# Kernel tuning notes

Measured on AMD Instinct MI355X. Metric: run time of the kernel, lower is better.

The kernel has to match this reference:

```python
import jax, jax.numpy as jnp
import numpy as np
import math

N_ENTITIES = 200000
N_ITEMS = 100000
N_REL = 40
DIM = 64
N_HEADS = 2
DK = DIM // N_HEADS
N_EDGES = 1500000
K_EDGES = 256
K_ITEMS = 100


def setup_inputs() -> dict:
    key = jax.random.key(0)
    k1, k2, k3, k4, k5, k6 = jax.random.split(key, 6)
    entity_emb = jax.random.normal(k1, (N_ENTITIES, DIM), jnp.float32) * 0.1
    W_Q = jax.random.normal(k2, (DIM, DIM), jnp.float32) * (1.0 / math.sqrt(DIM))
    relation_emb = jax.random.normal(k3, (N_REL - 1, DIM), jnp.float32) * 0.1
    edge_index = jax.random.randint(k4, (2, N_EDGES), 0, N_ENTITIES, jnp.int32)
    # edge_type in [1, N_REL-1]: code indexes relation_emb[edge_type - 1]
    edge_type = jax.random.randint(k5, (N_EDGES,), 1, N_REL, jnp.int32)
    # uniform(0,1) driving the gumbel noise -log(-log(u)); clipped away from 0
    noise_u = jax.random.uniform(k6, (N_EDGES,), jnp.float32, 1e-9, 1.0)
    return {"entity_emb": entity_emb, "W_Q": W_Q, "relation_emb": relation_emb,
            "noise_u": noise_u, "edge_index": edge_index, "edge_type": edge_type}


def reference(entity_emb, W_Q, relation_emb, noise_u, edge_index, edge_type):
    head, tail = edge_index[0], edge_index[1]
    E = edge_index.shape[1]

    # --- norm_attn_computer (AttnHGCN): per-edge multi-head attention ---
    # project once on nodes, then gather (same math as (emb[head] @ W_Q))
    proj = entity_emb @ W_Q                               # [N, D]
    q = proj[head].reshape(E, N_HEADS, DK)                # [E, H, Dk]
    k = proj[tail].reshape(E, N_HEADS, DK)                # [E, H, Dk]
    rel = relation_emb[edge_type - 1].reshape(E, N_HEADS, DK)
    attn = jnp.sum(q * k * rel, axis=-1) / math.sqrt(DK)  # [E, H]
    edge_attn_logits = attn.mean(axis=-1)                 # [E]

    # scatter_softmax over head nodes, then multiply by head degree (norm)
    seg_max = jax.lax.stop_gradient(
        jax.ops.segment_max(edge_attn_logits, head, num_segments=N_ENTITIES))
    ex = jnp.exp(edge_attn_logits - seg_max[head])
    denom = jax.ops.segment_sum(ex, head, num_segments=N_ENTITIES)
    edge_attn_score = ex / denom[head]
    deg = jax.ops.segment_sum(jnp.ones_like(edge_attn_logits), head,
                              num_segments=N_ENTITIES)
    edge_attn_score = edge_attn_score * deg[head]         # [E]

    # --- attn logit sums per item (head + tail scatter_sum), topk 100 ---
    sum_by_node = (jax.ops.segment_sum(edge_attn_logits, head, num_segments=N_ENTITIES)
                   + jax.ops.segment_sum(edge_attn_logits, tail, num_segments=N_ENTITIES))
    top_items_v, top_attn_items = jax.lax.top_k(sum_by_node[:N_ITEMS], K_ITEMS)

    # --- gumbel-noise injection + edge topk 256 ---
    noisy_score = edge_attn_score + (-jnp.log(-jnp.log(noise_u)))
    topk_v, topk_attn_edge_id = jax.lax.top_k(noisy_score, K_EDGES)

    return (edge_attn_score, topk_v, topk_attn_edge_id, top_items_v, top_attn_items)
```

## Files before the change

kernel.cpp:

```cpp
#include <hip/hip_runtime.h>

#define N_ENTITIES 200000
#define N_ITEMS    100000
#define DIM        64
#define N_EDGES    1500000
#define K_EDGES    256
#define K_ITEMS    100
#define SCALE      0.08838834764831845f

#define CAND_CAP   8192
#define NBLK3      1024

typedef unsigned long long u64;


__device__ __forceinline__ unsigned fkey(float x) {
    unsigned u = __float_as_uint(x);
    return (u & 0x80000000u) ? ~u : (u | 0x80000000u);
}
__device__ __forceinline__ float funkey(unsigned k) {
    return (k & 0x80000000u) ? __uint_as_float(k & 0x7fffffffu)
                             : __uint_as_float(~k);
}

__device__ __forceinline__ unsigned select_digit(const unsigned* __restrict__ hist,
                                                 unsigned Keff, unsigned* above) {
    unsigned cum = 0;
    int b = 255;
    for (; b > 0; --b) {
        unsigned hb = hist[b];
        if (cum + hb >= Keff) break;
        cum += hb;
    }
    *above = cum;
    return (unsigned)b;
}

__global__ __launch_bounds__(256) void proj_kernel(const float* __restrict__ emb,
                                                   const float* __restrict__ W,
                                                   float* __restrict__ proj,
                                                   const int* __restrict__ head,
                                                   float* __restrict__ ndf) {
    int e = blockIdx.x * blockDim.x + threadIdx.x;
    if (e < N_EDGES) atomicAdd(&ndf[2 * head[e] + 1], 1.0f);

    __shared__ float part[4][16][64];
    const int t = threadIdx.x;
    const int c = t & 63;
    const int q = __builtin_amdgcn_readfirstlane(t >> 6);

    float Wreg[16];
#pragma unroll
    for (int j = 0; j < 16; ++j) Wreg[j] = W[(q * 16 + j) * 64 + c];

    const int base = blockIdx.x * 16;
    const float* erow = emb + (size_t)base * 64 + q * 16;

    float acc[16];
#pragma unroll
    for (int r = 0; r < 16; ++r) acc[r] = 0.f;
#pragma unroll
    for (int r = 0; r < 16; ++r) {
#pragma unroll
        for (int j = 0; j < 16; ++j)
            acc[r] += erow[r * 64 + j] * Wreg[j];
    }
#pragma unroll
    for (int r = 0; r < 16; ++r) part[q][r][c] = acc[r];
    __syncthreads();
#pragma unroll
    for (int it = 0; it < 4; ++it) {
        int oi = t + it * 256;
        int r = oi >> 6, cc = oi & 63;
        float s = part[0][r][cc] + part[1][r][cc] + part[2][r][cc] + part[3][r][cc];
        proj[(size_t)(base + r) * 64 + cc] = s;
    }
}

__global__ __launch_bounds__(256) void edge_main(const float4* __restrict__ proj4,
                                                 const float4* __restrict__ rel4,
                                                 const int* __restrict__ head,
                                                 const int* __restrict__ tail,
                                                 const int* __restrict__ etype,
                                                 float* __restrict__ logits,
                                                 float* __restrict__ ndf,
                                                 float* __restrict__ sumI) {
    int wave = (blockIdx.x * blockDim.x + threadIdx.x) >> 6;
    int lane = threadIdx.x & 63;
    int slot = lane >> 4, sl = lane & 15;
    int ea = wave * 8 + slot, eb = ea + 4;

    int ha  = head[ea],  hb  = head[eb];
    int tta = tail[ea],  ttb = tail[eb];
    int ria = etype[ea] - 1, rib = etype[eb] - 1;

    float4 pha = proj4[(size_t)ha  * 16 + sl];
    float4 pta = proj4[(size_t)tta * 16 + sl];
    float4 qra = rel4[(size_t)ria * 16 + sl];
    float4 phb = proj4[(size_t)hb  * 16 + sl];
    float4 ptb = proj4[(size_t)ttb * 16 + sl];
    float4 qrb = rel4[(size_t)rib * 16 + sl];

    float xa = pha.x * pta.x * qra.x + pha.y * pta.y * qra.y
             + pha.z * pta.z * qra.z + pha.w * pta.w * qra.w;
    float xb = phb.x * ptb.x * qrb.x + phb.y * ptb.y * qrb.y
             + phb.z * ptb.z * qrb.z + phb.w * ptb.w * qrb.w;
    xa += __shfl_xor(xa, 1, 64);  xb += __shfl_xor(xb, 1, 64);
    xa += __shfl_xor(xa, 2, 64);  xb += __shfl_xor(xb, 2, 64);
    xa += __shfl_xor(xa, 4, 64);  xb += __shfl_xor(xb, 4, 64);
    xa += __shfl_xor(xa, 8, 64);  xb += __shfl_xor(xb, 8, 64);

    if (sl == 0) {
        float lga = xa * SCALE, lgb = xb * SCALE;
        logits[ea] = lga;
        logits[eb] = lgb;
        atomicAdd(&ndf[2 * ha], __expf(lga));
        atomicAdd(&ndf[2 * hb], __expf(lgb));
        if (ha  < N_ITEMS) atomicAdd(&sumI[ha],  lga);
        if (tta < N_ITEMS) atomicAdd(&sumI[tta], lga);
        if (hb  < N_ITEMS) atomicAdd(&sumI[hb],  lgb);
        if (ttb < N_ITEMS) atomicAdd(&sumI[ttb], lgb);
    }
}

__global__ __launch_bounds__(256) void edge_pass3(const float* __restrict__ logits,
                           const int* __restrict__ head,
                           const float* __restrict__ ndf, const float* __restrict__ noise_u,
                           const float* __restrict__ sumI,
                           float* __restrict__ out_scores, unsigned* __restrict__ keysE,
                           unsigned* __restrict__ keysI, unsigned* __restrict__ histB) {
    __shared__ unsigned hh[512];
    for (int j = threadIdx.x; j < 512; j += blockDim.x) hh[j] = 0;
    __syncthreads();

    const int stride = NBLK3 * 256;
    for (int i = blockIdx.x * blockDim.x + threadIdx.x; i < N_EDGES; i += stride) {
        float lg = logits[i];
        float2 dd = ((const float2*)ndf)[head[i]];
        float score = __expf(lg) / dd.x * dd.y;
        out_scores[i] = score;
        float noise = -logf(-logf(noise_u[i]));
        unsigned k = fkey(score + noise);
        keysE[i] = k;
        atomicAdd(&hh[k >> 24], 1u);
        if (i < N_ITEMS) {
            unsigned ki = fkey(sumI[i]);
            keysI[i] = ki;
            atomicAdd(&hh[256 + (ki >> 24)], 1u);
        }
    }
    __syncthreads();
    unsigned* row = histB + (size_t)blockIdx.x * 512;
    for (int j = threadIdx.x; j < 512; j += blockDim.x) row[j] = hh[j];
}

__global__ void reduce_hist_kernel(const unsigned* __restrict__ histB,
                                   unsigned* __restrict__ hists) {
    const int bin = blockIdx.x;
    unsigned s = 0;
    for (int r = threadIdx.x; r < NBLK3; r += 64)
        s += histB[(size_t)r * 512 + bin];
#pragma unroll
    for (int off = 1; off < 64; off <<= 1) s += __shfl_xor(s, off, 64);
    if (threadIdx.x == 0) hists[bin] = s;
}

__global__ void collect_kernel(const unsigned* __restrict__ keysE,
                               const unsigned* __restrict__ keysI,
                               const unsigned* __restrict__ hists,
                               unsigned* __restrict__ counters, unsigned* __restrict__ cand) {
    const int y = blockIdx.y;
    const unsigned* keys = y ? keysI : keysE;
    const int n = y ? N_ITEMS : N_EDGES;
    const unsigned K = y ? K_ITEMS : K_EDGES;
    const unsigned* H = hists + (size_t)y * 256;
    unsigned aboveA;
    unsigned binA = select_digit(H, K, &aboveA);
    const unsigned T = binA << 24;
    unsigned* cd = cand + (size_t)y * 2 * CAND_CAP;

    int i = blockIdx.x * blockDim.x + threadIdx.x;
    int stride = gridDim.x * blockDim.x;
    for (; i < n; i += stride) {
        unsigned k = keys[i];
        if (k >= T) {
            unsigned p = atomicAdd(&counters[y], 1u);
            if (p < (unsigned)CAND_CAP) { cd[2 * p] = k; cd[2 * p + 1] = (unsigned)i; }
        }
    }
}

__global__ void final_topk_kernel(const unsigned* __restrict__ cand,
                                  const unsigned* __restrict__ counters,
                                  float* __restrict__ out_topkv, float* __restrict__ out_topki,
                                  float* __restrict__ out_itemv, float* __restrict__ out_itemi) {
    __shared__ unsigned sk[CAND_CAP];
    __shared__ unsigned si[CAND_CAP];
    const int y = blockIdx.x;
    const int K = y ? K_ITEMS : K_EDGES;
    float* outv = y ? out_itemv : out_topkv;
    float* outi = y ? out_itemi : out_topki;
    const unsigned* cd = cand + (size_t)y * 2 * CAND_CAP;
    unsigned m = counters[y];
    if (m > (unsigned)CAND_CAP) m = CAND_CAP;
    for (unsigned i = threadIdx.x; i < m; i += blockDim.x) {
        sk[i] = cd[2 * i];
        si[i] = cd[2 * i + 1];
    }
    __syncthreads();
    for (unsigned i = threadIdx.x; i < m; i += blockDim.x) {
        unsigned ki = sk[i], xi = si[i];
        int r = 0;
        for (unsigned j = 0; j < m; ++j) {
            unsigned kj = sk[j];
            if (kj > ki || (kj == ki && si[j] < xi)) r++;
        }
        if (r < K) {
            outv[r] = funkey(ki);
            outi[r] = (float)xi;
        }
    }
}

extern "C" void kernel_launch(void* const* d_in, const int* in_sizes, int n_in,
                              void* d_out, int out_size, void* d_ws, size_t ws_size,
                              hipStream_t stream) {
    (void)in_sizes; (void)n_in; (void)out_size; (void)ws_size;
    const float* emb    = (const float*)d_in[0];
    const float* W      = (const float*)d_in[1];
    const float* rel    = (const float*)d_in[2];
    const float* noise  = (const float*)d_in[3];
    const int*   eidx   = (const int*)d_in[4];
    const int*   etype  = (const int*)d_in[5];
    const int* head = eidx;
    const int* tail = eidx + N_EDGES;

    float* out        = (float*)d_out;
    float* out_scores = out;
    float* out_topkv  = out + N_EDGES;
    float* out_topki  = out + N_EDGES + K_EDGES;
    float* out_itemv  = out + N_EDGES + 2 * K_EDGES;
    float* out_itemi  = out + N_EDGES + 2 * K_EDGES + K_ITEMS;

    float* ws = (float*)d_ws;
    size_t o = 0;
    float*    proj    = ws + o;               o += (size_t)N_ENTITIES * DIM;
    float*    ndf     = ws + o;               o += 2 * (size_t)N_ENTITIES;
    float*    sumI    = ws + o;               o += N_ITEMS;
    unsigned* counters= (unsigned*)(ws + o);  o += 2;
    float*    logits  = ws + o;               o += N_EDGES;
    unsigned* keysE   = (unsigned*)(ws + o);  o += N_EDGES;
    unsigned* keysI   = (unsigned*)(ws + o);  o += N_ITEMS;
    unsigned* histB   = (unsigned*)(ws + o);  o += (size_t)NBLK3 * 512;
    unsigned* hists   = (unsigned*)(ws + o);  o += 512;
    unsigned* cand    = (unsigned*)(ws + o);  o += 2 * 2 * CAND_CAP;

    hipMemsetAsync(ndf, 0, (2 * (size_t)N_ENTITIES + N_ITEMS + 2) * 4, stream);
    hipLaunchKernelGGL(proj_kernel, dim3(12500), dim3(256), 0, stream,
                       emb, W, proj, head, ndf);
    hipLaunchKernelGGL(edge_main, dim3(46875), dim3(256), 0, stream,
                       (const float4*)proj, (const float4*)rel, head, tail, etype,
                       logits, ndf, sumI);
    hipLaunchKernelGGL(edge_pass3, dim3(NBLK3), dim3(256), 0, stream,
                       logits, head, ndf, noise, sumI,
                       out_scores, keysE, keysI, histB);
    hipLaunchKernelGGL(reduce_hist_kernel, dim3(512), dim3(64), 0, stream, histB, hists);
    hipLaunchKernelGGL(collect_kernel, dim3(512, 2), dim3(256), 0, stream,
                       keysE, keysI, hists, counters, cand);
    hipLaunchKernelGGL(final_topk_kernel, dim3(2), dim3(1024), 0, stream,
                       cand, counters, out_topkv, out_topki, out_itemv, out_itemi);
}
```

Before: 476.1 us.

## Build head-sorted CSR via two-level bucket sort and process edges per node

Replaces per-edge processing with a counting sort of edges by head node: a two-level radix (bucket hist, scan, scatter, then per-bucket local sort in shared memory) produces a CSR of packed 64-bit edge records. A per-node wave kernel then loads the head projection once, computes logits for all outgoing edges, and accumulates softmax denominator, degree and head logit sums in registers instead of global atomics. This removes the head-indexed atomics and repeated head-row gathers, but adds five extra kernels and extra global traffic for the sort. Bucket capacity is clamped at L2CAP, so an unusually large bucket would silently drop edges.

```diff
diff --git a/kernel.cpp b/kernel.cpp
--- a/kernel.cpp
+++ b/kernel.cpp
@@ -10,6 +10,11 @@
 
 #define CAND_CAP   8192
 #define NBLK3      1024
+#define NB1        256
+#define EPB        5860
+#define NBUCK      782
+#define NSC        (NBUCK * NB1)
+#define L2CAP      2816
 
 typedef unsigned long long u64;
 
@@ -38,12 +43,7 @@
 
 __global__ __launch_bounds__(256) void proj_kernel(const float* __restrict__ emb,
                                                    const float* __restrict__ W,
-                                                   float* __restrict__ proj,
-                                                   const int* __restrict__ head,
-                                                   float* __restrict__ ndf) {
-    int e = blockIdx.x * blockDim.x + threadIdx.x;
-    if (e < N_EDGES) atomicAdd(&ndf[2 * head[e] + 1], 1.0f);
-
+                                                   float* __restrict__ proj) {
     __shared__ float part[4][16][64];
     const int t = threadIdx.x;
     const int c = t & 63;
@@ -77,56 +77,193 @@
     }
 }
 
-__global__ __launch_bounds__(256) void edge_main(const float4* __restrict__ proj4,
+__global__ __launch_bounds__(256) void bhist_kernel(const int* __restrict__ head,
+                                                    unsigned* __restrict__ off) {
+    __shared__ unsigned lh[NBUCK];
+    for (int k = threadIdx.x; k < NBUCK; k += 256) lh[k] = 0;
+    __syncthreads();
+    int base = blockIdx.x * EPB;
+    int end = base + EPB; if (end > N_EDGES) end = N_EDGES;
+    for (int e = base + threadIdx.x; e < end; e += 256)
+        atomicAdd(&lh[(unsigned)head[e] >> 8], 1u);
+    __syncthreads();
+    for (int k = threadIdx.x; k < NBUCK; k += 256)
+        off[(size_t)k * NB1 + blockIdx.x] = lh[k];
+}
+
+__global__ void scanA_kernel(unsigned* __restrict__ a, unsigned* __restrict__ bsum) {
+    __shared__ unsigned s[256];
+    int t = threadIdx.x, i = blockIdx.x * 256 + t;
+    unsigned v = a[i];
+    s[t] = v;
+    __syncthreads();
+    for (int off = 1; off < 256; off <<= 1) {
+        unsigned x = s[t];
+        unsigned y = (t >= off) ? s[t - off] : 0u;
+        __syncthreads();
+        s[t] = x + y;
+        __syncthreads();
+    }
+    a[i] = s[t] - v;
+    if (t == 255) bsum[blockIdx.x] = s[t];
+}
+__global__ __launch_bounds__(256) void scanB_kernel(const unsigned* __restrict__ bsum,
+                                                    unsigned* __restrict__ a) {
+    __shared__ unsigned part[4];
+    const int b = blockIdx.x;
+    const int t = threadIdx.x;
+    unsigned s = 0;
+    for (int j = t; j < b; j += 256) s += bsum[j];
+#pragma unroll
+    for (int off = 1; off < 64; off <<= 1) s += __shfl_xor(s, off, 64);
+    if ((t & 63) == 0) part[t >> 6] = s;
+    __syncthreads();
+    unsigned prefix = part[0] + part[1] + part[2] + part[3];
+    a[b * 256 + t] += prefix;
+}
+
+__global__ __launch_bounds__(256) void bscat_kernel(const int* __restrict__ head,
+                                                    const int* __restrict__ tail,
+                                                    const int* __restrict__ etype,
+                                                    const unsigned* __restrict__ off,
+                                                    u64* __restrict__ rec2) {
+    __shared__ unsigned lh[NBUCK];
+    __shared__ unsigned loff[NBUCK];
+    for (int k = threadIdx.x; k < NBUCK; k += 256) {
+        lh[k] = 0;
+        loff[k] = off[(size_t)k * NB1 + blockIdx.x];
+    }
+    __syncthreads();
+    int base = blockIdx.x * EPB;
+    int end = base + EPB; if (end > N_EDGES) end = N_EDGES;
+    for (int e = base + threadIdx.x; e < end; e += 256) {
+        unsigned h = (unsigned)head[e];
+        unsigned bkt = h >> 8;
+        unsigned r = atomicAdd(&lh[bkt], 1u);
+        u64 R = ((u64)h << 45) | ((u64)(unsigned)tail[e] << 27)
+              | ((u64)(unsigned)(etype[e] - 1) << 21) | (u64)(unsigned)e;
+        rec2[loff[bkt] + r] = R;
+    }
+}
+
+__global__ __launch_bounds__(256) void csr_kernel(const u64* __restrict__ rec2,
+                                                  const unsigned* __restrict__ off,
+                                                  u64* __restrict__ rec3,
+                                                  unsigned* __restrict__ start,
+                                                  unsigned* __restrict__ degtot) {
+    __shared__ u64 srec[L2CAP];
+    __shared__ u64 sdst[L2CAP];
+    __shared__ unsigned short srank[L2CAP];
+    __shared__ unsigned lh[256];
+    __shared__ unsigned lscan[256];
+    const int bkt = blockIdx.x;
+    const unsigned gstart = off[(size_t)bkt * NB1];
+    const unsigned gend = (bkt == NBUCK - 1) ? (unsigned)N_EDGES
+                                             : off[(size_t)(bkt + 1) * NB1];
+    unsigned n = gend - gstart;
+    if (n > L2CAP) n = L2CAP;
+    lh[threadIdx.x] = 0;
+    __syncthreads();
+    for (unsigned j = threadIdx.x; j < n; j += 256) {
+        u64 R = rec2[gstart + j];
+        srec[j] = R;
+        unsigned hl = (unsigned)(R >> 45) & 255u;
+        srank[j] = (unsigned short)atomicAdd(&lh[hl], 1u);
+    }
+    __syncthreads();
+    unsigned v = lh[threadIdx.x];
+    lscan[threadIdx.x] = v;
+    __syncthreads();
+    for (int o = 1; o < 256; o <<= 1) {
+        unsigned x = lscan[threadIdx.x];
+        unsigned y = (threadIdx.x >= o) ? lscan[threadIdx.x - o] : 0u;
+        __syncthreads();
+        lscan[threadIdx.x] = x + y;
+        __syncthreads();
+    }
+    unsigned excl = lscan[threadIdx.x] - v;
+    __syncthreads();
+    lscan[threadIdx.x] = excl;
+    const int h0 = bkt * 256;
+    const int entCount = (N_ENTITIES - h0 < 256) ? (N_ENTITIES - h0) : 256;
+    if ((int)threadIdx.x < entCount) {
+        start[h0 + threadIdx.x] = gstart + excl;
+        degtot[h0 + threadIdx.x] = v;
+    }
+    __syncthreads();
+    for (unsigned j = threadIdx.x; j < n; j += 256) {
+        u64 R = srec[j];
+        unsigned hl = (unsigned)(R >> 45) & 255u;
+        sdst[lscan[hl] + srank[j]] = R;
+    }
+    __syncthreads();
+    for (unsigned j = threadIdx.x; j < n; j += 256) rec3[gstart + j] = sdst[j];
+}
+
+__global__ __launch_bounds__(256) void node_pass(const float4* __restrict__ proj4,
                                                  const float4* __restrict__ rel4,
-                                                 const int* __restrict__ head,
-                                                 const int* __restrict__ tail,
-                                                 const int* __restrict__ etype,
+                                                 const u64* __restrict__ rec,
+                                                 const unsigned* __restrict__ start,
+                                                 const unsigned* __restrict__ degtot,
                                                  float* __restrict__ logits,
-                                                 float* __restrict__ ndf,
+                                                 float2* __restrict__ nd,
+                                                 float* __restrict__ sumhead,
                                                  float* __restrict__ sumI) {
     int wave = (blockIdx.x * blockDim.x + threadIdx.x) >> 6;
     int lane = threadIdx.x & 63;
     int slot = lane >> 4, sl = lane & 15;
-    int ea = wave * 8 + slot, eb = ea + 4;
-
-    int ha  = head[ea],  hb  = head[eb];
-    int tta = tail[ea],  ttb = tail[eb];
-    int ria = etype[ea] - 1, rib = etype[eb] - 1;
-
-    float4 pha = proj4[(size_t)ha  * 16 + sl];
-    float4 pta = proj4[(size_t)tta * 16 + sl];
-    float4 qra = rel4[(size_t)ria * 16 + sl];
-    float4 phb = proj4[(size_t)hb  * 16 + sl];
-    float4 ptb = proj4[(size_t)ttb * 16 + sl];
-    float4 qrb = rel4[(size_t)rib * 16 + sl];
-
-    float xa = pha.x * pta.x * qra.x + pha.y * pta.y * qra.y
-             + pha.z * pta.z * qra.z + pha.w * pta.w * qra.w;
-    float xb = phb.x * ptb.x * qrb.x + phb.y * ptb.y * qrb.y
-             + phb.z * ptb.z * qrb.z + phb.w * ptb.w * qrb.w;
-    xa += __shfl_xor(xa, 1, 64);  xb += __shfl_xor(xb, 1, 64);
-    xa += __shfl_xor(xa, 2, 64);  xb += __shfl_xor(xb, 2, 64);
-    xa += __shfl_xor(xa, 4, 64);  xb += __shfl_xor(xb, 4, 64);
-    xa += __shfl_xor(xa, 8, 64);  xb += __shfl_xor(xb, 8, 64);
-
-    if (sl == 0) {
-        float lga = xa * SCALE, lgb = xb * SCALE;
-        logits[ea] = lga;
-        logits[eb] = lgb;
-        atomicAdd(&ndf[2 * ha], __expf(lga));
-        atomicAdd(&ndf[2 * hb], __expf(lgb));
-        if (ha  < N_ITEMS) atomicAdd(&sumI[ha],  lga);
-        if (tta < N_ITEMS) atomicAdd(&sumI[tta], lga);
-        if (hb  < N_ITEMS) atomicAdd(&sumI[hb],  lgb);
-        if (ttb < N_ITEMS) atomicAdd(&sumI[ttb], lgb);
+    unsigned s = start[wave], len = degtot[wave];
+    float4 ph = proj4[(size_t)wave * 16 + sl];
+    float dsum = 0.f, lsum = 0.f;
+    for (unsigned k0 = 0; k0 < len; k0 += 8) {
+        unsigned ka = k0 + slot, kb = ka + 4;
+        bool va = (ka < len), vb = (kb < len);
+        u64 Ra = rec[s + (va ? ka : 0u)];
+        u64 Rb = rec[s + (vb ? kb : 0u)];
+        unsigned ta = (unsigned)(Ra >> 27) & 0x3FFFFu, ria = ((unsigned)(Ra >> 21)) & 63u;
+        unsigned tb = (unsigned)(Rb >> 27) & 0x3FFFFu, rib = ((unsigned)(Rb >> 21)) & 63u;
+        unsigned ea = (unsigned)Ra & 0x1FFFFFu, eb = (unsigned)Rb & 0x1FFFFFu;
+        float4 pa = proj4[(size_t)ta * 16 + sl];
+        float4 qa = rel4[(size_t)ria * 16 + sl];
+        float4 pb = proj4[(size_t)tb * 16 + sl];
+        float4 qb = rel4[(size_t)rib * 16 + sl];
+        float xa = ph.x * pa.x * qa.x + ph.y * pa.y * qa.y + ph.z * pa.z * qa.z + ph.w * pa.w * qa.w;
+        float xb = ph.x * pb.x * qb.x + ph.y * pb.y * qb.y + ph.z * pb.z * qb.z + ph.w * pb.w * qb.w;
+        xa += __shfl_xor(xa, 1, 64);  xb += __shfl_xor(xb, 1, 64);
+        xa += __shfl_xor(xa, 2, 64);  xb += __shfl_xor(xb, 2, 64);
+        xa += __shfl_xor(xa, 4, 64);  xb += __shfl_xor(xb, 4, 64);
+        xa += __shfl_xor(xa, 8, 64);  xb += __shfl_xor(xb, 8, 64);
+        if (sl == 0) {
+            if (va) {
+                float lg = xa * SCALE;
+                logits[ea] = lg;
+                dsum += __expf(lg);
+                lsum += lg;
+                if (ta < N_ITEMS) atomicAdd(&sumI[ta], lg);
+            }
+            if (vb) {
+                float lg = xb * SCALE;
+                logits[eb] = lg;
+                dsum += __expf(lg);
+                lsum += lg;
+                if (tb < N_ITEMS) atomicAdd(&sumI[tb], lg);
+            }
+        }
+    }
+    dsum += __shfl_xor(dsum, 16, 64);
+    dsum += __shfl_xor(dsum, 32, 64);
+    lsum += __shfl_xor(lsum, 16, 64);
+    lsum += __shfl_xor(lsum, 32, 64);
+    if (lane == 0) {
+        nd[wave] = make_float2(dsum, (float)len);
+        sumhead[wave] = lsum;
     }
 }
 
 __global__ __launch_bounds__(256) void edge_pass3(const float* __restrict__ logits,
                            const int* __restrict__ head,
-                           const float* __restrict__ ndf, const float* __restrict__ noise_u,
-                           const float* __restrict__ sumI,
+                           const float2* __restrict__ nd, const float* __restrict__ noise_u,
+                           const float* __restrict__ sumhead, const float* __restrict__ sumI,
                            float* __restrict__ out_scores, unsigned* __restrict__ keysE,
                            unsigned* __restrict__ keysI, unsigned* __restrict__ histB) {
     __shared__ unsigned hh[512];
@@ -136,7 +273,7 @@
     const int stride = NBLK3 * 256;
     for (int i = blockIdx.x * blockDim.x + threadIdx.x; i < N_EDGES; i += stride) {
         float lg = logits[i];
-        float2 dd = ((const float2*)ndf)[head[i]];
+        float2 dd = nd[head[i]];
         float score = __expf(lg) / dd.x * dd.y;
         out_scores[i] = score;
         float noise = -logf(-logf(noise_u[i]));
@@ -144,7 +281,7 @@
         keysE[i] = k;
         atomicAdd(&hh[k >> 24], 1u);
         if (i < N_ITEMS) {
-            unsigned ki = fkey(sumI[i]);
+            unsigned ki = fkey(sumhead[i] + sumI[i]);
             keysI[i] = ki;
             atomicAdd(&hh[256 + (ki >> 24)], 1u);
         }
@@ -245,24 +382,37 @@
     float* ws = (float*)d_ws;
     size_t o = 0;
     float*    proj    = ws + o;               o += (size_t)N_ENTITIES * DIM;
-    float*    ndf     = ws + o;               o += 2 * (size_t)N_ENTITIES;
+    unsigned* off     = (unsigned*)(ws + o);  o += NSC;
+    unsigned* bsum    = (unsigned*)(ws + o);  o += 1024;
+    u64*      rec2    = (u64*)(ws + o);       o += 2 * (size_t)N_EDGES;
+    u64*      rec3    = (u64*)(ws + o);       o += 2 * (size_t)N_EDGES;
+    unsigned* keysE   = (unsigned*)rec2;
+    unsigned* keysI   = keysE + N_EDGES;
+    unsigned* start   = (unsigned*)(ws + o);  o += N_ENTITIES;
+    unsigned* degtot  = (unsigned*)(ws + o);  o += N_ENTITIES;
+    float*    logits  = ws + o;               o += N_EDGES;
+    float2*   nd      = (float2*)(ws + o);    o += 2 * (size_t)N_ENTITIES;
+    float*    sumhead = ws + o;               o += N_ENTITIES;
     float*    sumI    = ws + o;               o += N_ITEMS;
     unsigned* counters= (unsigned*)(ws + o);  o += 2;
-    float*    logits  = ws + o;               o += N_EDGES;
-    unsigned* keysE   = (unsigned*)(ws + o);  o += N_EDGES;
-    unsigned* keysI   = (unsigned*)(ws + o);  o += N_ITEMS;
     unsigned* histB   = (unsigned*)(ws + o);  o += (size_t)NBLK3 * 512;
     unsigned* hists   = (unsigned*)(ws + o);  o += 512;
     unsigned* cand    = (unsigned*)(ws + o);  o += 2 * 2 * CAND_CAP;
 
-    hipMemsetAsync(ndf, 0, (2 * (size_t)N_ENTITIES + N_ITEMS + 2) * 4, stream);
-    hipLaunchKernelGGL(proj_kernel, dim3(12500), dim3(256), 0, stream,
-                       emb, W, proj, head, ndf);
-    hipLaunchKernelGGL(edge_main, dim3(46875), dim3(256), 0, stream,
-                       (const float4*)proj, (const float4*)rel, head, tail, etype,
-                       logits, ndf, sumI);
+    hipMemsetAsync(sumI, 0, ((size_t)N_ITEMS + 2) * 4, stream);
+    hipLaunchKernelGGL(proj_kernel, dim3(12500), dim3(256), 0, stream, emb, W, proj);
+    hipLaunchKernelGGL(bhist_kernel, dim3(NB1), dim3(256), 0, stream, head, off);
+    hipLaunchKernelGGL(scanA_kernel, dim3(NSC / 256), dim3(256), 0, stream, off, bsum);
+    hipLaunchKernelGGL(scanB_kernel, dim3(NSC / 256), dim3(256), 0, stream, bsum, off);
+    hipLaunchKernelGGL(bscat_kernel, dim3(NB1), dim3(256), 0, stream,
+                       head, tail, etype, off, rec2);
+    hipLaunchKernelGGL(csr_kernel, dim3(NBUCK), dim3(256), 0, stream,
+                       rec2, off, rec3, start, degtot);
+    hipLaunchKernelGGL(node_pass, dim3(N_ENTITIES / 4), dim3(256), 0, stream,
+                       (const float4*)proj, (const float4*)rel, rec3, start, degtot,
+                       logits, nd, sumhead, sumI);
     hipLaunchKernelGGL(edge_pass3, dim3(NBLK3), dim3(256), 0, stream,
-                       logits, head, ndf, noise, sumI,
+                       logits, head, nd, noise, sumhead, sumI,
                        out_scores, keysE, keysI, histB);
     hipLaunchKernelGGL(reduce_hist_kernel, dim3(512), dim3(64), 0, stream, histB, hists);
     hipLaunchKernelGGL(collect_kernel, dim3(512, 2), dim3(256), 0, stream,
```

Measured after the change: 437.1 us. -8.2%, faster.
